# Performance work log

Hardware: AMD Instinct MI355X
Metric: run time of the kernel (lower is better)

Reference implementation:

```python
import jax, jax.numpy as jnp
import numpy as np

HID, HEADS, FF, DEPTH = 1152, 16, 4304, 2
HD = HID // HEADS            # 72
ROT = HD // 2                # 36 (rotary_pos_emb width)
S, NSEG = 2048, 4
EPS = 1e-6


def _layernorm(x, w, b):
    m = jnp.mean(x, axis=-1, keepdims=True)
    xc = x - m
    v = jnp.mean(xc * xc, axis=-1, keepdims=True)
    return xc * jax.lax.rsqrt(v + EPS) * w + b


def _rotate_half(x):
    x1, x2 = jnp.split(x, 2, axis=-1)
    return jnp.concatenate([-x2, x1], axis=-1)


def _apply_rotary(t, freqs):
    # t: [S, H, D], freqs: [S, D/2]
    emb = jnp.concatenate([freqs, freqs], axis=-1)          # [S, D]
    cos = jnp.cos(emb)[:, None, :]
    sin = jnp.sin(emb)[:, None, :]
    return t * cos + _rotate_half(t) * sin


def setup_inputs() -> dict:
    key = jax.random.key(0)
    ks = jax.random.split(key, 16)
    sd = 0.02
    # rotary freqs as in VisionRotaryEmbedding(dim=HD//2): h-pos and w-pos halves
    inv_freq = 1.0 / (10000.0 ** (jnp.arange(0, ROT, 2, dtype=jnp.float32) / ROT))  # [18]
    pos = jnp.arange(S, dtype=jnp.float32)
    hpos, wpos = pos // 32.0, pos % 32.0
    rotary = jnp.concatenate([jnp.outer(hpos, inv_freq), jnp.outer(wpos, inv_freq)], axis=-1)  # [S, 36]
    return {
        "x": jax.random.normal(ks[0], (S, HID), jnp.float32),
        "cu_seqlens": jnp.arange(NSEG + 1, dtype=jnp.int32) * (S // NSEG),
        "rotary_pos_emb": rotary,
        "norm1_w": jnp.ones((DEPTH, HID), jnp.float32),
        "norm1_b": jnp.zeros((DEPTH, HID), jnp.float32),
        "qkv_w": jax.random.normal(ks[1], (DEPTH, 3 * HID, HID), jnp.float32) * sd,
        "qkv_b": jnp.zeros((DEPTH, 3 * HID), jnp.float32),
        "proj_w": jax.random.normal(ks[2], (DEPTH, HID, HID), jnp.float32) * sd,
        "proj_b": jnp.zeros((DEPTH, HID), jnp.float32),
        "norm2_w": jnp.ones((DEPTH, HID), jnp.float32),
        "norm2_b": jnp.zeros((DEPTH, HID), jnp.float32),
        "fc1_w": jax.random.normal(ks[3], (DEPTH, FF, HID), jnp.float32) * sd,
        "fc1_b": jnp.zeros((DEPTH, FF), jnp.float32),
        "fc2_w": jax.random.normal(ks[4], (DEPTH, HID, FF), jnp.float32) * sd,
        "fc2_b": jnp.zeros((DEPTH, HID), jnp.float32),
    }


def _forward(x, cu_seqlens, rotary_pos_emb, norm1_w, norm1_b, qkv_w, qkv_b,
             proj_w, proj_b, norm2_w, norm2_b, fc1_w, fc1_b, fc2_w, fc2_b):
    seq_len = x.shape[0]
    # block-diagonal additive mask from cu_seqlens (same mask the torch loop builds)
    seg = jnp.searchsorted(cu_seqlens, jnp.arange(seq_len, dtype=cu_seqlens.dtype), side="right") - 1
    same = seg[:, None] == seg[None, :]
    bias = jnp.where(same, jnp.float32(0.0), jnp.finfo(jnp.float32).min)  # [S, S]
    scale = 1.0 / np.sqrt(HD)
    for d in range(DEPTH):
        # --- attention ---
        h = _layernorm(x, norm1_w[d], norm1_b[d])
        qkv = (h @ qkv_w[d].T + qkv_b[d]).reshape(seq_len, 3, HEADS, HD)
        q, k, v = qkv[:, 0], qkv[:, 1], qkv[:, 2]           # [S, H, D]
        q = _apply_rotary(q, rotary_pos_emb)
        k = _apply_rotary(k, rotary_pos_emb)
        scores = jnp.einsum("qhd,khd->hqk", q, k) * scale + bias[None]
        probs = jax.nn.softmax(scores.astype(jnp.float32), axis=-1).astype(q.dtype)
        attn = jnp.einsum("hqk,khd->qhd", probs, v).reshape(seq_len, HID)
        x = x + attn @ proj_w[d].T + proj_b[d]
        # --- MLP (gelu tanh approx) ---
        h2 = _layernorm(x, norm2_w[d], norm2_b[d])
        x = x + jax.nn.gelu(h2 @ fc1_w[d].T + fc1_b[d], approximate=True) @ fc2_w[d].T + fc2_b[d]
    return x


def reference(x, cu_seqlens, rotary_pos_emb, norm1_w, norm1_b, qkv_w, qkv_b,
              proj_w, proj_b, norm2_w, norm2_b, fc1_w, fc1_b, fc2_w, fc2_b):
    return _forward(x, cu_seqlens, rotary_pos_emb, norm1_w, norm1_b, qkv_w, qkv_b,
                    proj_w, proj_b, norm2_w, norm2_b, fc1_w, fc1_b, fc2_w, fc2_b)
```

## Files before the change

### kernel.cpp

```cpp
#include <hip/hip_runtime.h>

#define S_LEN 2048
#define HID   1152
#define HEADS 16
#define HD    72
#define ROT   36
#define LD3   3456
#define FF    4304
#define FFP   4320

typedef short s16x8 __attribute__((ext_vector_type(8)));
typedef short s16x4 __attribute__((ext_vector_type(4)));
typedef float f32x4 __attribute__((ext_vector_type(4)));
typedef short bf_t;

__device__ __forceinline__ short f2b(float f) {
  unsigned u = __float_as_uint(f);
  u += 0x7fffu + ((u >> 16) & 1u);
  return (short)(u >> 16);
}
__device__ __forceinline__ float b2f(short h) {
  return __uint_as_float(((unsigned)(unsigned short)h) << 16);
}
__device__ __forceinline__ float gelu_f(float x) {
  float t = tanhf(0.7978845608028654f * (x + 0.044715f * x * x * x));
  return 0.5f * x * (1.0f + t);
}

typedef const __attribute__((address_space(1))) void* gas_p;
typedef __attribute__((address_space(3))) void* las_p;
__device__ __forceinline__ void gload16(const void* g, void* l) {
  __builtin_amdgcn_global_load_lds((gas_p)g, (las_p)l, 16, 0, 0);
}

__global__ __launch_bounds__(256) void convw4_kernel(
    const float* __restrict__ src, int N, int K,
    bf_t* __restrict__ dst, int Kpad)
{
  int idx = blockIdx.x * 256 + threadIdx.x;
  int kq = Kpad >> 2;
  if (idx >= N * kq) return;
  int n = idx / kq, k = (idx % kq) << 2;
  s16x4 o;
  if (k + 3 < K) {
    float4 v = *(const float4*)(src + (size_t)n * K + k);
    o[0] = f2b(v.x); o[1] = f2b(v.y); o[2] = f2b(v.z); o[3] = f2b(v.w);
  } else {
#pragma unroll
    for (int j = 0; j < 4; j++) {
      int kk = k + j;
      o[j] = (kk < K) ? f2b(src[(size_t)n * K + kk]) : (short)0;
    }
  }
  *(s16x4*)(dst + (size_t)n * Kpad + k) = o;
}

__global__ __launch_bounds__(256) void costab_kernel(
    const float* __restrict__ rot, float* __restrict__ ct, float* __restrict__ st)
{
  int i = blockIdx.x * 256 + threadIdx.x;
  if (i < S_LEN * ROT) { float f = rot[i]; ct[i] = cosf(f); st[i] = sinf(f); }
}

__global__ __launch_bounds__(256) void ln_kernel(
    const float* __restrict__ x, const float* __restrict__ wgt,
    const float* __restrict__ bia, bf_t* __restrict__ outb)
{
  const int row = blockIdx.x, tid = threadIdx.x;
  const float4* xr = (const float4*)(x + (size_t)row * HID);
  float4 a = xr[tid];
  float4 b2 = make_float4(0.f, 0.f, 0.f, 0.f);
  const bool has2 = tid < 32;
  if (has2) b2 = xr[256 + tid];
  float s = a.x + a.y + a.z + a.w + b2.x + b2.y + b2.z + b2.w;
  float q = a.x*a.x + a.y*a.y + a.z*a.z + a.w*a.w
          + b2.x*b2.x + b2.y*b2.y + b2.z*b2.z + b2.w*b2.w;
  for (int mk = 32; mk; mk >>= 1) { s += __shfl_xor(s, mk); q += __shfl_xor(q, mk); }
  __shared__ float red[16];
  if ((tid & 63) == 0) { red[tid >> 6] = s; red[8 + (tid >> 6)] = q; }
  __syncthreads();
  if (tid == 0) {
    red[4]  = red[0] + red[1] + red[2] + red[3];
    red[12] = red[8] + red[9] + red[10] + red[11];
  }
  __syncthreads();
  float mean = red[4] * (1.0f / HID);
  float var  = red[12] * (1.0f / HID) - mean * mean;
  float rstd = rsqrtf(var + 1e-6f);
  const float4* w4 = (const float4*)wgt;
  const float4* b4 = (const float4*)bia;
  s16x4* o4 = (s16x4*)(outb + (size_t)row * HID);
  {
    float4 wv = w4[tid], bv = b4[tid];
    s16x4 o;
    o[0] = f2b((a.x - mean) * rstd * wv.x + bv.x);
    o[1] = f2b((a.y - mean) * rstd * wv.y + bv.y);
    o[2] = f2b((a.z - mean) * rstd * wv.z + bv.z);
    o[3] = f2b((a.w - mean) * rstd * wv.w + bv.w);
    o4[tid] = o;
  }
  if (has2) {
    float4 wv = w4[256 + tid], bv = b4[256 + tid];
    s16x4 o;
    o[0] = f2b((b2.x - mean) * rstd * wv.x + bv.x);
    o[1] = f2b((b2.y - mean) * rstd * wv.y + bv.y);
    o[2] = f2b((b2.z - mean) * rstd * wv.z + bv.z);
    o[3] = f2b((b2.w - mean) * rstd * wv.w + bv.w);
    o4[256 + tid] = o;
  }
}

__global__ __launch_bounds__(256) void rotary_kernel(
    bf_t* __restrict__ qkv, const float* __restrict__ ct, const float* __restrict__ st)
{
  int idx = blockIdx.x * 256 + threadIdx.x;
  if (idx >= S_LEN * HEADS * ROT) return;
  int t = idx / (HEADS * ROT);
  int r = idx % (HEADS * ROT);
  int h = r / ROT, dd = r % ROT;
  float c = ct[t * ROT + dd], s = st[t * ROT + dd];
  size_t base = (size_t)t * LD3 + h * HD + dd;
  float q1 = b2f(qkv[base]),        q2 = b2f(qkv[base + ROT]);
  float k1 = b2f(qkv[base + HID]),  k2 = b2f(qkv[base + HID + ROT]);
  const float scale = 0.11785113019775793f;
  qkv[base]             = f2b((q1 * c - q2 * s) * scale);
  qkv[base + ROT]       = f2b((q2 * c + q1 * s) * scale);
  qkv[base + HID]       = f2b(k1 * c - k2 * s);
  qkv[base + HID + ROT] = f2b(k2 * c + k1 * s);
}

template<int MODE>
__global__ __launch_bounds__(256, 4) void gemm3(
    const bf_t* __restrict__ A, int lda,
    const bf_t* __restrict__ B, int ldb,
    const float* __restrict__ bias, int nbias,
    void* outp, int ldc, int nvalid, int K, int kchunk)
{
  __shared__ __align__(16) bf_t As[2][128 * 32];
  __shared__ __align__(16) bf_t Bs[2][128 * 32];
  const int tid = threadIdx.x;
  const int l = tid & 63, w = tid >> 6;
  const int lr = l & 15, lg = l >> 4;
  const int wm = (w >> 1) * 64, wn = (w & 1) * 64;

  unsigned gx = gridDim.x, gy = gridDim.y, gz = gridDim.z;
  unsigned nwg = gx * gy * gz;
  unsigned lin = (blockIdx.z * gy + blockIdx.y) * gx + blockIdx.x;
  if ((nwg & 7u) == 0u) {
    unsigned q = nwg >> 3;
    lin = (lin & 7u) * q + (lin >> 3);
  }
  const unsigned bz = lin / (gx * gy);
  const unsigned rem = lin % (gx * gy);
  const unsigned by = rem / gx, bx = rem % gx;

  const int rowA0 = by * 128, colB0 = bx * 128;
  const int kb0 = bz * kchunk;
  int kb1 = kb0 + kchunk; if (kb1 > K) kb1 = K;

  const int o1 = tid * 16, o2 = o1 + 4096;
  const int r1 = o1 >> 6, c1 = o1 & 63;
  const int r2 = r1 + 64;
  const char* Ab = (const char*)A;
  const char* Bb = (const char*)B;

#define STAGE(buf, kk) do { \
    gload16(Ab + ((size_t)(rowA0 + r1) * lda + (kk)) * 2 + c1, (char*)As[buf] + o1); \
    gload16(Ab + ((size_t)(rowA0 + r2) * lda + (kk)) * 2 + c1, (char*)As[buf] + o2); \
    gload16(Bb + ((size_t)(colB0 + r1) * ldb + (kk)) * 2 + c1, (char*)Bs[buf] + o1); \
    gload16(Bb + ((size_t)(colB0 + r2) * ldb + (kk)) * 2 + c1, (char*)Bs[buf] + o2); \
  } while (0)

  f32x4 acc[4][4] = {};

  STAGE(0, kb0);
  asm volatile("s_waitcnt vmcnt(0)" ::: "memory");
  __builtin_amdgcn_s_barrier();
  __builtin_amdgcn_sched_barrier(0);

  int cur = 0;
  for (int kb = kb0; kb < kb1; kb += 32) {
    if (kb + 32 < kb1) STAGE(cur ^ 1, kb + 32);
    s16x8 af[4], bv[4];
#pragma unroll
    for (int mt = 0; mt < 4; mt++)
      af[mt] = *(const s16x8*)&As[cur][(wm + mt * 16 + lr) * 32 + lg * 8];
#pragma unroll
    for (int nt = 0; nt < 4; nt++)
      bv[nt] = *(const s16x8*)&Bs[cur][(wn + nt * 16 + lr) * 32 + lg * 8];
    asm volatile("s_waitcnt lgkmcnt(0)" ::: "memory");
    __builtin_amdgcn_sched_barrier(0);
#pragma unroll
    for (int mt = 0; mt < 4; mt++)
#pragma unroll
      for (int nt = 0; nt < 4; nt++)
        acc[mt][nt] = __builtin_amdgcn_mfma_f32_16x16x32_bf16(af[mt], bv[nt], acc[mt][nt], 0, 0, 0);
    asm volatile("s_waitcnt vmcnt(0)" ::: "memory");
    __builtin_amdgcn_s_barrier();
    __builtin_amdgcn_sched_barrier(0);
    cur ^= 1;
  }
#undef STAGE

#pragma unroll
  for (int mt = 0; mt < 4; mt++) {
    const int rr = rowA0 + wm + mt * 16 + lg * 4;
#pragma unroll
    for (int nt = 0; nt < 4; nt++) {
      const int cc = colB0 + wn + nt * 16 + lr;
      const float bvl = (cc < nbias) ? bias[cc] : 0.0f;
#pragma unroll
      for (int i = 0; i < 4; i++) {
        float v = acc[mt][nt][i] + bvl;
        const int row = rr + i;
        if (MODE == 0) {
          ((bf_t*)outp)[(size_t)row * ldc + cc] = f2b(v);
        } else if (MODE == 2) {
          if (cc < nvalid)      ((bf_t*)outp)[(size_t)row * ldc + cc] = f2b(gelu_f(v));
          else if (cc < ldc)    ((bf_t*)outp)[(size_t)row * ldc + cc] = 0;
        } else {
          float* P = (float*)outp + (size_t)bz * ((size_t)S_LEN * ldc);
          P[(size_t)row * ldc + cc] = v;
        }
      }
    }
  }
}

__global__ __launch_bounds__(256) void reduce_kernel(
    const float* __restrict__ part, const float* __restrict__ bias,
    const float* __restrict__ resid, float* __restrict__ outp)
{
  int idx = blockIdx.x * 256 + threadIdx.x;
  if (idx >= S_LEN * HID / 4) return;
  float4 r = ((const float4*)resid)[idx];
  float4 bv = ((const float4*)bias)[idx % (HID / 4)];
  float sx = r.x + bv.x, sy = r.y + bv.y, sz = r.z + bv.z, sw = r.w + bv.w;
#pragma unroll
  for (int p = 0; p < 4; p++) {
    float4 v = ((const float4*)(part + (size_t)p * S_LEN * HID))[idx];
    sx += v.x; sy += v.y; sz += v.z; sw += v.w;
  }
  ((float4*)outp)[idx] = make_float4(sx, sy, sz, sw);
}

#define QSTR 104
#define VSTR 72
#define PSTR 72
__global__ __launch_bounds__(256, 2) void attn_kernel(
    const bf_t* __restrict__ qkv, const int* __restrict__ cu, int nseg,
    bf_t* __restrict__ outb)
{
  __shared__ __align__(16) bf_t Qs[64 * QSTR];
  __shared__ __align__(16) bf_t Ks[64 * QSTR];
  __shared__ __align__(16) bf_t VTs[80 * VSTR];
  __shared__ __align__(16) bf_t Pb[4][16 * PSTR];
  const int tid = threadIdx.x;
  const int l = tid & 63, w = tid >> 6;
  const int lr = l & 15, lg = l >> 4;
  const int h = blockIdx.y;
  const int qbase = blockIdx.x * 64;

  int kstart = 0, kend = S_LEN;
  for (int s2 = 0; s2 < nseg; s2++) {
    int a = cu[s2], b = cu[s2 + 1];
    if (qbase >= a && qbase < b) { kstart = a; kend = b; }
  }

  for (int i = tid; i < 64 * QSTR; i += 256)
    if ((i % QSTR) >= HD) { Qs[i] = 0; Ks[i] = 0; }
  for (int i = tid; i < 80 * VSTR; i += 256)
    if ((i / VSTR) >= HD) VTs[i] = 0;
  for (int c = tid; c < 576; c += 256) {
    int r = c / 9, j = c % 9;
    *(s16x8*)&Qs[r * QSTR + j * 8] =
        *(const s16x8*)&qkv[(size_t)(qbase + r) * LD3 + h * HD + j * 8];
  }
  __syncthreads();
  s16x8 qf[3];
#pragma unroll
  for (int ks = 0; ks < 3; ks++)
    qf[ks] = *(const s16x8*)&Qs[(w * 16 + lr) * QSTR + ks * 32 + lg * 8];

  float m_i[4], l_i[4];
  f32x4 Of[5] = {};
#pragma unroll
  for (int i = 0; i < 4; i++) { m_i[i] = -1e30f; l_i[i] = 0.0f; }

  for (int kb = kstart; kb < kend; kb += 64) {
    __syncthreads();
    for (int c = tid; c < 576; c += 256) {
      int r = c / 9, j = c % 9;
      int gr = kb + r; if (gr >= kend) gr = kend - 1;
      *(s16x8*)&Ks[r * QSTR + j * 8] =
          *(const s16x8*)&qkv[(size_t)gr * LD3 + HID + h * HD + j * 8];
    }
    for (int c = tid; c < 576; c += 256) {
      int r = c / 9, j = c % 9;
      int gr = kb + r; if (gr >= kend) gr = kend - 1;
      s16x8 v = *(const s16x8*)&qkv[(size_t)gr * LD3 + 2 * HID + h * HD + j * 8];
#pragma unroll
      for (int jj = 0; jj < 8; jj++) VTs[(j * 8 + jj) * VSTR + r] = v[jj];
    }
    __syncthreads();

    f32x4 sc[4] = {};
#pragma unroll
    for (int kc = 0; kc < 4; kc++) {
#pragma unroll
      for (int ks = 0; ks < 3; ks++) {
        s16x8 kf = *(const s16x8*)&Ks[(kc * 16 + lr) * QSTR + ks * 32 + lg * 8];
        sc[kc] = __builtin_amdgcn_mfma_f32_16x16x32_bf16(qf[ks], kf, sc[kc], 0, 0, 0);
      }
    }
#pragma unroll
    for (int kc = 0; kc < 4; kc++) {
      if ((kb + kc * 16 + lr) >= kend) {
#pragma unroll
        for (int i = 0; i < 4; i++) sc[kc][i] = -1e30f;
      }
    }
    float tmax[4], scl[4], rs[4];
#pragma unroll
    for (int i = 0; i < 4; i++) {
      float t = fmaxf(fmaxf(sc[0][i], sc[1][i]), fmaxf(sc[2][i], sc[3][i]));
#pragma unroll
      for (int d2 = 1; d2 < 16; d2 <<= 1) t = fmaxf(t, __shfl_xor(t, d2));
      tmax[i] = t;
    }
#pragma unroll
    for (int i = 0; i < 4; i++) {
      float mn = fmaxf(m_i[i], tmax[i]);
      scl[i] = __expf(m_i[i] - mn);
      m_i[i] = mn;
      rs[i] = 0.0f;
    }
#pragma unroll
    for (int kc = 0; kc < 4; kc++)
#pragma unroll
      for (int i = 0; i < 4; i++) {
        float p = __expf(sc[kc][i] - m_i[i]);
        sc[kc][i] = p;
        rs[i] += p;
      }
#pragma unroll
    for (int i = 0; i < 4; i++) {
#pragma unroll
      for (int d2 = 1; d2 < 16; d2 <<= 1) rs[i] += __shfl_xor(rs[i], d2);
      l_i[i] = l_i[i] * scl[i] + rs[i];
    }
#pragma unroll
    for (int nt = 0; nt < 5; nt++)
#pragma unroll
      for (int i = 0; i < 4; i++) Of[nt][i] *= scl[i];
#pragma unroll
    for (int kc = 0; kc < 4; kc++)
#pragma unroll
      for (int i = 0; i < 4; i++)
        Pb[w][(lg * 4 + i) * PSTR + kc * 16 + lr] = f2b(sc[kc][i]);
    __syncthreads();
    s16x8 pf[2];
#pragma unroll
    for (int k2 = 0; k2 < 2; k2++)
      pf[k2] = *(const s16x8*)&Pb[w][lr * PSTR + k2 * 32 + lg * 8];
#pragma unroll
    for (int nt = 0; nt < 5; nt++) {
#pragma unroll
      for (int k2 = 0; k2 < 2; k2++) {
        s16x8 vf = *(const s16x8*)&VTs[(nt * 16 + lr) * VSTR + k2 * 32 + lg * 8];
        Of[nt] = __builtin_amdgcn_mfma_f32_16x16x32_bf16(pf[k2], vf, Of[nt], 0, 0, 0);
      }
    }
  }
  float inv[4];
#pragma unroll
  for (int i = 0; i < 4; i++) inv[i] = 1.0f / l_i[i];
#pragma unroll
  for (int nt = 0; nt < 5; nt++) {
    int cc = nt * 16 + lr;
    if (cc < HD) {
#pragma unroll
      for (int i = 0; i < 4; i++) {
        int row = qbase + w * 16 + lg * 4 + i;
        outb[(size_t)row * HID + h * HD + cc] = f2b(Of[nt][i] * inv[i]);
      }
    }
  }
}

extern "C" void kernel_launch(void* const* d_in, const int* in_sizes, int n_in,
                              void* d_out, int out_size, void* d_ws, size_t ws_size,
                              hipStream_t stream) {
  const float* x     = (const float*)d_in[0];
  const int*   cu    = (const int*)d_in[1];
  const float* rotab = (const float*)d_in[2];
  const float* n1w   = (const float*)d_in[3];
  const float* n1b   = (const float*)d_in[4];
  const float* qkvw  = (const float*)d_in[5];
  const float* qkvb  = (const float*)d_in[6];
  const float* projw = (const float*)d_in[7];
  const float* projb = (const float*)d_in[8];
  const float* n2w   = (const float*)d_in[9];
  const float* n2b   = (const float*)d_in[10];
  const float* fc1w  = (const float*)d_in[11];
  const float* fc1b  = (const float*)d_in[12];
  const float* fc2w  = (const float*)d_in[13];
  const float* fc2b  = (const float*)d_in[14];
  float* out = (float*)d_out;
  char* ws = (char*)d_ws;

  size_t off = 0;
  float* xbuf = (float*)(ws + off); off += (size_t)S_LEN * HID * 4;
  bf_t* hbf   = (bf_t*)(ws + off);  off += (size_t)S_LEN * HID * 2;
  bf_t* qkvbf = (bf_t*)(ws + off);
  bf_t* ff1bf = (bf_t*)(ws + off);  off += (size_t)S_LEN * FFP * 2;
  bf_t* attnbf= (bf_t*)(ws + off);  off += (size_t)S_LEN * HID * 2;
  bf_t* wslot = (bf_t*)(ws + off);  off += (size_t)4352 * 1152 * 2;
  float* ctab = (float*)(ws + off); off += (size_t)S_LEN * ROT * 4;
  float* stab = (float*)(ws + off); off += (size_t)S_LEN * ROT * 4;
  float* part = (float*)(ws + off); off += (size_t)4 * S_LEN * HID * 4;

  costab_kernel<<<(S_LEN * ROT + 255) / 256, 256, 0, stream>>>(rotab, ctab, stab);

  const int nseg = in_sizes[1] - 1;
  const int RED_GRID = (S_LEN * HID / 4 + 255) / 256;

  for (int d = 0; d < 2; d++) {
    const float* xin = (d == 0) ? x : xbuf;
    ln_kernel<<<S_LEN, 256, 0, stream>>>(xin, n1w + d * HID, n1b + d * HID, hbf);
    convw4_kernel<<<(LD3 * HID / 4 + 255) / 256, 256, 0, stream>>>(
        qkvw + (size_t)d * LD3 * HID, LD3, HID, wslot, HID);
    gemm3<0><<<dim3(LD3 / 128, 16), 256, 0, stream>>>(
        hbf, HID, wslot, HID, qkvb + (size_t)d * LD3, LD3, qkvbf, LD3, LD3, HID, HID);
    rotary_kernel<<<(S_LEN * HEADS * ROT + 255) / 256, 256, 0, stream>>>(qkvbf, ctab, stab);
    attn_kernel<<<dim3(S_LEN / 64, HEADS), 256, 0, stream>>>(qkvbf, cu, nseg, attnbf);
    convw4_kernel<<<(HID * HID / 4 + 255) / 256, 256, 0, stream>>>(
        projw + (size_t)d * HID * HID, HID, HID, wslot, HID);
    gemm3<3><<<dim3(HID / 128, 16, 4), 256, 0, stream>>>(
        attnbf, HID, wslot, HID, nullptr, 0, part, HID, HID, HID, 288);
    reduce_kernel<<<RED_GRID, 256, 0, stream>>>(part, projb + (size_t)d * HID, xin, xbuf);
    ln_kernel<<<S_LEN, 256, 0, stream>>>(xbuf, n2w + d * HID, n2b + d * HID, hbf);
    convw4_kernel<<<(FF * HID / 4 + 255) / 256, 256, 0, stream>>>(
        fc1w + (size_t)d * FF * HID, FF, HID, wslot, HID);
    gemm3<2><<<dim3(4352 / 128, 16), 256, 0, stream>>>(
        hbf, HID, wslot, HID, fc1b + (size_t)d * FF, FF, ff1bf, FFP, FF, HID, HID);
    convw4_kernel<<<(HID * FFP / 4 + 255) / 256, 256, 0, stream>>>(
        fc2w + (size_t)d * HID * FF, HID, FF, wslot, FFP);
    gemm3<3><<<dim3(HID / 128, 16, 4), 256, 0, stream>>>(
        ff1bf, FFP, wslot, FFP, nullptr, 0, part, HID, HID, FFP, 1088);
    float* outp = (d == 1) ? out : xbuf;
    reduce_kernel<<<RED_GRID, 256, 0, stream>>>(part, fc2b + (size_t)d * HID, xbuf, outp);
  }
}
```

Before: 458.5 us.

## Add 128x64 tile GEMM with BK=64 for QKV and FC1 projections

Adds a new gemm4 kernel that uses 128x64 output tiles with a K-step of 64 and swizzled LDS, and uses it for the QKV and FC1 GEMMs in place of the 128x128, K=32 gemm3. The smaller N tile doubles the workgroup count, which should fill the CUs better (QKV goes from 432 to 864 blocks). The deeper K step halves the number of barriers per tile. gemm3 is trimmed to the split-K fp32 partial-output path only. The trade-off is less operand reuse per tile and higher LDS use per block, with occupancy bounded at 3.

```diff
diff --git a/kernel.cpp b/kernel.cpp
--- a/kernel.cpp
+++ b/kernel.cpp
@@ -130,6 +130,103 @@
 }
 
 template<int MODE>
+__global__ __launch_bounds__(256, 3) void gemm4(
+    const bf_t* __restrict__ A, int lda,
+    const bf_t* __restrict__ B, int ldb,
+    const float* __restrict__ bias, int nbias,
+    void* outp, int ldc, int nvalid, int K)
+{
+  __shared__ __align__(16) bf_t As[2][128 * 64];
+  __shared__ __align__(16) bf_t Bs[2][64 * 64];
+  const int tid = threadIdx.x;
+  const int l = tid & 63, w = tid >> 6;
+  const int lr = l & 15, lg = l >> 4;
+  const int wm = (w >> 1) * 64, wn = (w & 1) * 32;
+
+  unsigned gx = gridDim.x, gy = gridDim.y;
+  unsigned nwg = gx * gy;
+  unsigned lin = blockIdx.y * gx + blockIdx.x;
+  if ((nwg & 7u) == 0u) { unsigned q = nwg >> 3; lin = (lin & 7u) * q + (lin >> 3); }
+  const unsigned by = lin / gx, bx = lin % gx;
+
+  const int rowA0 = by * 128, colB0 = bx * 64;
+
+  const int rS = tid >> 3;
+  const int cS = ((tid & 7) * 16) ^ ((rS & 7) << 4);
+  const char* Ab = (const char*)A;
+  const char* Bb = (const char*)B;
+
+#define STAGE4(buf, kk) do { \
+    _Pragma("unroll") \
+    for (int j = 0; j < 4; j++) \
+      gload16(Ab + ((size_t)(rowA0 + j * 32 + rS) * lda + (kk)) * 2 + cS, \
+              (char*)As[buf] + j * 4096 + tid * 16); \
+    _Pragma("unroll") \
+    for (int j = 0; j < 2; j++) \
+      gload16(Bb + ((size_t)(colB0 + j * 32 + rS) * ldb + (kk)) * 2 + cS, \
+              (char*)Bs[buf] + j * 4096 + tid * 16); \
+  } while (0)
+
+  f32x4 acc[4][2] = {};
+
+  STAGE4(0, 0);
+  asm volatile("s_waitcnt vmcnt(0)" ::: "memory");
+  __builtin_amdgcn_s_barrier();
+  __builtin_amdgcn_sched_barrier(0);
+
+  int cur = 0;
+  for (int kb = 0; kb < K; kb += 64) {
+    if (kb + 64 < K) STAGE4(cur ^ 1, kb + 64);
+    s16x8 af[2][4], bv[2][2];
+#pragma unroll
+    for (int kk = 0; kk < 2; kk++) {
+      const int cb = (kk * 64 + lg * 16) ^ ((lr & 7) << 4);
+#pragma unroll
+      for (int mt = 0; mt < 4; mt++)
+        af[kk][mt] = *(const s16x8*)((const char*)&As[cur][0] + (wm + mt * 16 + lr) * 128 + cb);
+#pragma unroll
+      for (int nt = 0; nt < 2; nt++)
+        bv[kk][nt] = *(const s16x8*)((const char*)&Bs[cur][0] + (wn + nt * 16 + lr) * 128 + cb);
+    }
+    asm volatile("s_waitcnt lgkmcnt(0)" ::: "memory");
+    __builtin_amdgcn_sched_barrier(0);
+#pragma unroll
+    for (int kk = 0; kk < 2; kk++)
+#pragma unroll
+      for (int mt = 0; mt < 4; mt++)
+#pragma unroll
+        for (int nt = 0; nt < 2; nt++)
+          acc[mt][nt] = __builtin_amdgcn_mfma_f32_16x16x32_bf16(af[kk][mt], bv[kk][nt], acc[mt][nt], 0, 0, 0);
+    asm volatile("s_waitcnt vmcnt(0)" ::: "memory");
+    __builtin_amdgcn_s_barrier();
+    __builtin_amdgcn_sched_barrier(0);
+    cur ^= 1;
+  }
+#undef STAGE4
+
+#pragma unroll
+  for (int mt = 0; mt < 4; mt++) {
+    const int rr = rowA0 + wm + mt * 16 + lg * 4;
+#pragma unroll
+    for (int nt = 0; nt < 2; nt++) {
+      const int cc = colB0 + wn + nt * 16 + lr;
+      const float bvl = (cc < nbias) ? bias[cc] : 0.0f;
+#pragma unroll
+      for (int i = 0; i < 4; i++) {
+        float v = acc[mt][nt][i] + bvl;
+        const int row = rr + i;
+        if (MODE == 0) {
+          ((bf_t*)outp)[(size_t)row * ldc + cc] = f2b(v);
+        } else {
+          if (cc < nvalid)      ((bf_t*)outp)[(size_t)row * ldc + cc] = f2b(gelu_f(v));
+          else if (cc < ldc)    ((bf_t*)outp)[(size_t)row * ldc + cc] = 0;
+        }
+      }
+    }
+  }
+}
+
+template<int MODE>
 __global__ __launch_bounds__(256, 4) void gemm3(
     const bf_t* __restrict__ A, int lda,
     const bf_t* __restrict__ B, int ldb,
@@ -208,20 +305,11 @@
 #pragma unroll
     for (int nt = 0; nt < 4; nt++) {
       const int cc = colB0 + wn + nt * 16 + lr;
-      const float bvl = (cc < nbias) ? bias[cc] : 0.0f;
 #pragma unroll
       for (int i = 0; i < 4; i++) {
-        float v = acc[mt][nt][i] + bvl;
         const int row = rr + i;
-        if (MODE == 0) {
-          ((bf_t*)outp)[(size_t)row * ldc + cc] = f2b(v);
-        } else if (MODE == 2) {
-          if (cc < nvalid)      ((bf_t*)outp)[(size_t)row * ldc + cc] = f2b(gelu_f(v));
-          else if (cc < ldc)    ((bf_t*)outp)[(size_t)row * ldc + cc] = 0;
-        } else {
-          float* P = (float*)outp + (size_t)bz * ((size_t)S_LEN * ldc);
-          P[(size_t)row * ldc + cc] = v;
-        }
+        float* P = (float*)outp + (size_t)bz * ((size_t)S_LEN * ldc);
+        P[(size_t)row * ldc + cc] = acc[mt][nt][i];
       }
     }
   }
@@ -430,8 +518,8 @@
     ln_kernel<<<S_LEN, 256, 0, stream>>>(xin, n1w + d * HID, n1b + d * HID, hbf);
     convw4_kernel<<<(LD3 * HID / 4 + 255) / 256, 256, 0, stream>>>(
         qkvw + (size_t)d * LD3 * HID, LD3, HID, wslot, HID);
-    gemm3<0><<<dim3(LD3 / 128, 16), 256, 0, stream>>>(
-        hbf, HID, wslot, HID, qkvb + (size_t)d * LD3, LD3, qkvbf, LD3, LD3, HID, HID);
+    gemm4<0><<<dim3(LD3 / 64, 16), 256, 0, stream>>>(
+        hbf, HID, wslot, HID, qkvb + (size_t)d * LD3, LD3, qkvbf, LD3, LD3, HID);
     rotary_kernel<<<(S_LEN * HEADS * ROT + 255) / 256, 256, 0, stream>>>(qkvbf, ctab, stab);
     attn_kernel<<<dim3(S_LEN / 64, HEADS), 256, 0, stream>>>(qkvbf, cu, nseg, attnbf);
     convw4_kernel<<<(HID * HID / 4 + 255) / 256, 256, 0, stream>>>(
@@ -442,8 +530,8 @@
     ln_kernel<<<S_LEN, 256, 0, stream>>>(xbuf, n2w + d * HID, n2b + d * HID, hbf);
     convw4_kernel<<<(FF * HID / 4 + 255) / 256, 256, 0, stream>>>(
         fc1w + (size_t)d * FF * HID, FF, HID, wslot, HID);
-    gemm3<2><<<dim3(4352 / 128, 16), 256, 0, stream>>>(
-        hbf, HID, wslot, HID, fc1b + (size_t)d * FF, FF, ff1bf, FFP, FF, HID, HID);
+    gemm4<2><<<dim3(4352 / 64, 16), 256, 0, stream>>>(
+        hbf, HID, wslot, HID, fc1b + (size_t)d * FF, FF, ff1bf, FFP, FF, HID);
     convw4_kernel<<<(HID * FFP / 4 + 255) / 256, 256, 0, stream>>>(
         fc2w + (size_t)d * HID * FF, HID, FF, wslot, FFP);
     gemm3<3><<<dim3(HID / 128, 16, 4), 256, 0, stream>>>(
```

Measured after the change: 466.1 us. No clear change (+1.7%).

## Use split-K with a reduce kernel for QKV, FC1 and FC2 GEMMs

Applied to the files above, without the earlier changes.

Splits the K dimension of the QKV and FC1 GEMMs in two, and of FC2 in eight, writing fp32 partials. A templated reduce kernel sums the partials and applies bias, plus GELU or the residual where needed, with bf16 or fp32 output. FFP is padded to 4352 so FC2 splits evenly. The aim is more workgroups for better CU occupancy, at the cost of extra fp32 partial traffic and additional reduce launches. The new path is used only when the workspace is large enough, otherwise the old single-pass GEMMs run.

```diff
diff --git a/kernel.cpp b/kernel.cpp
--- a/kernel.cpp
+++ b/kernel.cpp
@@ -7,7 +7,7 @@
 #define ROT   36
 #define LD3   3456
 #define FF    4304
-#define FFP   4320
+#define FFP   4352
 
 typedef short s16x8 __attribute__((ext_vector_type(8)));
 typedef short s16x4 __attribute__((ext_vector_type(4)));
@@ -208,7 +208,7 @@
 #pragma unroll
     for (int nt = 0; nt < 4; nt++) {
       const int cc = colB0 + wn + nt * 16 + lr;
-      const float bvl = (cc < nbias) ? bias[cc] : 0.0f;
+      const float bvl = (MODE == 3) ? 0.0f : ((cc < nbias) ? bias[cc] : 0.0f);
 #pragma unroll
       for (int i = 0; i < 4; i++) {
         float v = acc[mt][nt][i] + bvl;
@@ -227,21 +227,43 @@
   }
 }
 
-__global__ __launch_bounds__(256) void reduce_kernel(
-    const float* __restrict__ part, const float* __restrict__ bias,
-    const float* __restrict__ resid, float* __restrict__ outp)
+template<int RMODE>
+__global__ __launch_bounds__(256) void reduceT(
+    const float* __restrict__ part, int np, const float* __restrict__ bias,
+    const float* __restrict__ resid, void* __restrict__ outp,
+    int ldc, int nvalid)
 {
   int idx = blockIdx.x * 256 + threadIdx.x;
-  if (idx >= S_LEN * HID / 4) return;
-  float4 r = ((const float4*)resid)[idx];
-  float4 bv = ((const float4*)bias)[idx % (HID / 4)];
-  float sx = r.x + bv.x, sy = r.y + bv.y, sz = r.z + bv.z, sw = r.w + bv.w;
-#pragma unroll
-  for (int p = 0; p < 4; p++) {
-    float4 v = ((const float4*)(part + (size_t)p * S_LEN * HID))[idx];
+  int tot = S_LEN * (ldc >> 2);
+  if (idx >= tot) return;
+  int col4 = idx % (ldc >> 2);
+  int col = col4 << 2;
+  float sx = 0.f, sy = 0.f, sz = 0.f, sw = 0.f;
+  for (int p = 0; p < np; p++) {
+    float4 v = ((const float4*)(part + (size_t)p * S_LEN * ldc))[idx];
     sx += v.x; sy += v.y; sz += v.z; sw += v.w;
   }
-  ((float4*)outp)[idx] = make_float4(sx, sy, sz, sw);
+  if (RMODE == 0) {
+    float4 bv = ((const float4*)bias)[col4];
+    s16x4 o;
+    o[0] = f2b(sx + bv.x); o[1] = f2b(sy + bv.y);
+    o[2] = f2b(sz + bv.z); o[3] = f2b(sw + bv.w);
+    ((s16x4*)outp)[idx] = o;
+  } else if (RMODE == 1) {
+    float4 r = ((const float4*)resid)[idx];
+    float4 bv = ((const float4*)bias)[col4];
+    ((float4*)outp)[idx] = make_float4(r.x + bv.x + sx, r.y + bv.y + sy,
+                                       r.z + bv.z + sz, r.w + bv.w + sw);
+  } else {
+    float vv[4] = {sx, sy, sz, sw};
+    s16x4 o;
+#pragma unroll
+    for (int j = 0; j < 4; j++) {
+      int cc = col + j;
+      o[j] = (cc < nvalid) ? f2b(gelu_f(vv[j] + bias[cc])) : (short)0;
+    }
+    ((s16x4*)outp)[idx] = o;
+  }
 }
 
 #define QSTR 104
@@ -415,40 +437,69 @@
   bf_t* qkvbf = (bf_t*)(ws + off);
   bf_t* ff1bf = (bf_t*)(ws + off);  off += (size_t)S_LEN * FFP * 2;
   bf_t* attnbf= (bf_t*)(ws + off);  off += (size_t)S_LEN * HID * 2;
-  bf_t* wslot = (bf_t*)(ws + off);  off += (size_t)4352 * 1152 * 2;
+  bf_t* wslot = (bf_t*)(ws + off);  off += (size_t)HID * FFP * 2;
   float* ctab = (float*)(ws + off); off += (size_t)S_LEN * ROT * 4;
   float* stab = (float*)(ws + off); off += (size_t)S_LEN * ROT * 4;
-  float* part = (float*)(ws + off); off += (size_t)4 * S_LEN * HID * 4;
+  float* part = (float*)(ws + off);
+  size_t need_big   = off + (size_t)8 * S_LEN * HID * 4;
+  size_t need_big2  = off + (size_t)2 * S_LEN * FFP * 4;
+  if (need_big2 > need_big) need_big = need_big2;
+  const bool big = ws_size >= need_big;
 
   costab_kernel<<<(S_LEN * ROT + 255) / 256, 256, 0, stream>>>(rotab, ctab, stab);
 
   const int nseg = in_sizes[1] - 1;
-  const int RED_GRID = (S_LEN * HID / 4 + 255) / 256;
+  const int RED_H   = (S_LEN * HID / 4 + 255) / 256;
+  const int RED_Q   = (S_LEN * LD3 / 4 + 255) / 256;
+  const int RED_F   = (S_LEN * FFP / 4 + 255) / 256;
 
   for (int d = 0; d < 2; d++) {
     const float* xin = (d == 0) ? x : xbuf;
     ln_kernel<<<S_LEN, 256, 0, stream>>>(xin, n1w + d * HID, n1b + d * HID, hbf);
     convw4_kernel<<<(LD3 * HID / 4 + 255) / 256, 256, 0, stream>>>(
         qkvw + (size_t)d * LD3 * HID, LD3, HID, wslot, HID);
-    gemm3<0><<<dim3(LD3 / 128, 16), 256, 0, stream>>>(
-        hbf, HID, wslot, HID, qkvb + (size_t)d * LD3, LD3, qkvbf, LD3, LD3, HID, HID);
+    if (big) {
+      gemm3<3><<<dim3(LD3 / 128, 16, 2), 256, 0, stream>>>(
+          hbf, HID, wslot, HID, nullptr, 0, part, LD3, LD3, HID, 576);
+      reduceT<0><<<RED_Q, 256, 0, stream>>>(
+          part, 2, qkvb + (size_t)d * LD3, nullptr, qkvbf, LD3, LD3);
+    } else {
+      gemm3<0><<<dim3(LD3 / 128, 16), 256, 0, stream>>>(
+          hbf, HID, wslot, HID, qkvb + (size_t)d * LD3, LD3, qkvbf, LD3, LD3, HID, HID);
+    }
     rotary_kernel<<<(S_LEN * HEADS * ROT + 255) / 256, 256, 0, stream>>>(qkvbf, ctab, stab);
     attn_kernel<<<dim3(S_LEN / 64, HEADS), 256, 0, stream>>>(qkvbf, cu, nseg, attnbf);
     convw4_kernel<<<(HID * HID / 4 + 255) / 256, 256, 0, stream>>>(
         projw + (size_t)d * HID * HID, HID, HID, wslot, HID);
     gemm3<3><<<dim3(HID / 128, 16, 4), 256, 0, stream>>>(
         attnbf, HID, wslot, HID, nullptr, 0, part, HID, HID, HID, 288);
-    reduce_kernel<<<RED_GRID, 256, 0, stream>>>(part, projb + (size_t)d * HID, xin, xbuf);
+    reduceT<1><<<RED_H, 256, 0, stream>>>(
+        part, 4, projb + (size_t)d * HID, xin, xbuf, HID, HID);
     ln_kernel<<<S_LEN, 256, 0, stream>>>(xbuf, n2w + d * HID, n2b + d * HID, hbf);
     convw4_kernel<<<(FF * HID / 4 + 255) / 256, 256, 0, stream>>>(
         fc1w + (size_t)d * FF * HID, FF, HID, wslot, HID);
-    gemm3<2><<<dim3(4352 / 128, 16), 256, 0, stream>>>(
-        hbf, HID, wslot, HID, fc1b + (size_t)d * FF, FF, ff1bf, FFP, FF, HID, HID);
+    if (big) {
+      gemm3<3><<<dim3(FFP / 128, 16, 2), 256, 0, stream>>>(
+          hbf, HID, wslot, HID, nullptr, 0, part, FFP, FF, HID, 576);
+      reduceT<2><<<RED_F, 256, 0, stream>>>(
+          part, 2, fc1b + (size_t)d * FF, nullptr, ff1bf, FFP, FF);
+    } else {
+      gemm3<2><<<dim3(FFP / 128, 16), 256, 0, stream>>>(
+          hbf, HID, wslot, HID, fc1b + (size_t)d * FF, FF, ff1bf, FFP, FF, HID, HID);
+    }
     convw4_kernel<<<(HID * FFP / 4 + 255) / 256, 256, 0, stream>>>(
         fc2w + (size_t)d * HID * FF, HID, FF, wslot, FFP);
-    gemm3<3><<<dim3(HID / 128, 16, 4), 256, 0, stream>>>(
-        ff1bf, FFP, wslot, FFP, nullptr, 0, part, HID, HID, FFP, 1088);
     float* outp = (d == 1) ? out : xbuf;
-    reduce_kernel<<<RED_GRID, 256, 0, stream>>>(part, fc2b + (size_t)d * HID, xbuf, outp);
-  }
-}
+    if (big) {
+      gemm3<3><<<dim3(HID / 128, 16, 8), 256, 0, stream>>>(
+          ff1bf, FFP, wslot, FFP, nullptr, 0, part, HID, HID, FFP, 576);
+      reduceT<1><<<RED_H, 256, 0, stream>>>(
+          part, 8, fc2b + (size_t)d * HID, xbuf, outp, HID, HID);
+    } else {
+      gemm3<3><<<dim3(HID / 128, 16, 4), 256, 0, stream>>>(
+          ff1bf, FFP, wslot, FFP, nullptr, 0, part, HID, HID, FFP, 1088);
+      reduceT<1><<<RED_H, 256, 0, stream>>>(
+          part, 4, fc2b + (size_t)d * HID, xbuf, outp, HID, HID);
+    }
+  }
+}
```

Result: slower. 522.0 us (+13.8%).
